# Optimization experiments

Hardware: AMD Instinct MI355X
Metric: run time of the kernel (lower is better)

The kernel has to match this reference:

```python
import jax, jax.numpy as jnp
import numpy as np

B, L, H, N, O = 64, 512, 768, 50, 768
ALPHA = 0.3  # leaky relu slope in GAT
NEG_INF = -9e15


def _position_encoding(n, d):
    # standard sinusoidal PE, shape [n, d]
    pos = jnp.arange(n, dtype=jnp.float32)[:, None]              # [n,1]
    div = jnp.exp(jnp.arange(0, d, 2, dtype=jnp.float32) * (-np.log(10000.0) / d))  # [d/2]
    ang = pos * div[None, :]                                     # [n, d/2]
    return jnp.stack([jnp.sin(ang), jnp.cos(ang)], axis=-1).reshape(n, d)


def _gat_layer(x, adj, W, b, a, ab):
    # Dense GAT layer. Original builds an [N,N,2F] concat tensor then applies
    # linear a; mathematically identical to splitting a into src/dst halves.
    Wh = x @ W + b                                               # [N,F]
    Fdim = Wh.shape[-1]
    a_src = Wh @ a[:Fdim]                                        # [N]
    a_dst = Wh @ a[Fdim:]                                        # [N]
    e = jax.nn.leaky_relu(a_src[:, None] + a_dst[None, :] + ab, negative_slope=ALPHA)
    att = jax.nn.softmax(jnp.where(adj > 0, e, NEG_INF), axis=1)  # rows sum to 1
    return att @ Wh                                              # [N,F]


def setup_inputs() -> dict:
    key = jax.random.key(0)
    ks = jax.random.split(key, 16)
    s = 1.0 / np.sqrt(H)
    utter_embedding = jax.random.normal(ks[0], (B, L, H), jnp.float32)
    cls_ids = jnp.sort(jax.random.randint(ks[1], (B, N), 0, L), axis=1).astype(jnp.int32)
    adj = jax.random.randint(ks[2], (B, N, N), 0, 2).astype(jnp.int32)
    adj = adj | jnp.eye(N, dtype=jnp.int32)  # ensure self loops so softmax rows are valid
    return {
        "utter_embedding": utter_embedding,
        "cls_ids": cls_ids,
        "adj": adj,
        # GAT head 0 (concat=True)
        "W1": jax.random.normal(ks[3], (H, H), jnp.float32) * s,
        "b1": jnp.zeros((H,), jnp.float32),
        "a1": jax.random.normal(ks[4], (2 * H,), jnp.float32) * s,
        "ab1": jnp.zeros((), jnp.float32),
        # GAT out layer (concat=False)
        "W2": jax.random.normal(ks[5], (H, H), jnp.float32) * s,
        "b2": jnp.zeros((H,), jnp.float32),
        "a2": jax.random.normal(ks[6], (2 * H,), jnp.float32) * s,
        "ab2": jnp.zeros((), jnp.float32),
        # Attention pooling over utterances
        "Wa": jax.random.normal(ks[7], (H, H), jnp.float32) * s,
        "ba": jnp.zeros((H,), jnp.float32),
        "v": jax.random.normal(ks[8], (H,), jnp.float32) * s,
        # Final linear
        "Wl": jax.random.normal(ks[9], (H, O), jnp.float32) * s,
        "bl": jnp.zeros((O,), jnp.float32),
    }


def reference(utter_embedding, cls_ids, adj, W1, b1, a1, ab1, W2, b2, a2, ab2,
              Wa, ba, v, Wl, bl):
    pe = _position_encoding(N, H)                                # [N,H]

    def per_dialogue(emb, ids, A):
        # gather [CLS] utterance embeddings: index_select
        x = jnp.take(emb, ids, axis=0)                           # [N,H]
        x = x + pe                                               # position encoder
        # GAT: 1 head concat -> elu, out layer -> elu, residual
        h = jax.nn.elu(_gat_layer(x, A, W1, b1, a1, ab1))
        h = jax.nn.elu(_gat_layer(h, A, W2, b2, a2, ab2)) + x    # residual per GAT.forward
        # attention pooling over N utterances
        scores = jax.nn.softmax(jnp.tanh(h @ Wa + ba) @ v, axis=0)  # [N]
        return scores @ h                                        # [H]

    dialogue = jax.vmap(per_dialogue)(utter_embedding, cls_ids, adj)  # [B,H]
    return dialogue @ Wl + bl                                    # [B,O]
```

## Files before the change

kernel.cpp:

```cpp
#include <hip/hip_runtime.h>
#include <hip/hip_bf16.h>
#include <math.h>

typedef __attribute__((ext_vector_type(8))) short bf16x8;
typedef __attribute__((ext_vector_type(4))) float f32x4;
typedef __attribute__((ext_vector_type(4))) unsigned short u16x4;

constexpr int Bn = 64;
constexpr int Ln = 512;
constexpr int Hd = 768;
constexpr int Nn = 50;
constexpr int On = 768;
constexpr int RP = 64;

__device__ __forceinline__ f32x4 MFMA(bf16x8 a, bf16x8 b, f32x4 c) {
  return __builtin_amdgcn_mfma_f32_16x16x32_bf16(a, b, c, 0, 0, 0);
}
__device__ __forceinline__ unsigned short f2bb(float v) {
  __hip_bfloat16 h = __float2bfloat16(v);
  return *(unsigned short*)&h;
}

struct PrepArgs {
  const float* src[4];
  __hip_bfloat16* dst[4];
  const float* emb;
  const int* ids;
  float* xres;
  __hip_bfloat16* xb;
  float* aux;
};

__global__ __launch_bounds__(256) void prep_kernel(PrepArgs a) {
  int bx = blockIdx.x;
  if (bx < 2304) {
    __shared__ float tile[32][33];
    int job = bx / 576, t = bx % 576;
    const float* W = a.src[job];
    __hip_bfloat16* Wt = a.dst[job];
    int tx = (t % 24) * 32, ty = (t / 24) * 32;
    int c = threadIdx.x & 31, r0 = threadIdx.x >> 5;
    for (int r = r0; r < 32; r += 8)
      tile[r][c] = W[(size_t)(tx + r) * Hd + ty + c];
    __syncthreads();
    for (int r = r0; r < 32; r += 8)
      Wt[(size_t)(ty + r) * Hd + tx + c] = __float2bfloat16(tile[c][r]);
  } else if (bx < 6400) {
    int bn = bx - 2304;
    int b = bn >> 6, i = bn & 63;
    __hip_bfloat16* xbo = a.xb + (size_t)bn * Hd;
    float* xro = a.xres + (size_t)bn * Hd;
    if (i < Nn) {
      int id = a.ids[b * Nn + i];
      const float* src = a.emb + ((size_t)b * Ln + id) * Hd;
      const float kLog = 9.210340371976184f / (float)Hd;
      for (int h = threadIdx.x; h < Hd; h += 256) {
        float freq = expf(-(float)(h & ~1) * kLog);
        float ang = (float)i * freq;
        float v = src[h] + ((h & 1) ? cosf(ang) : sinf(ang));
        xbo[h] = __float2bfloat16(v);
        xro[h] = v;
      }
    } else {
      for (int h = threadIdx.x; h < Hd; h += 256) {
        xbo[h] = __float2bfloat16(0.f);
        xro[h] = 0.f;
      }
    }
  } else {
    int idx = (bx - 6400) * 256 + threadIdx.x;
    if (idx < 5 * Bn * RP) a.aux[idx] = 0.f;
  }
}

template <int EPI>
__global__ __launch_bounds__(256) void gemm_kernel(
    const __hip_bfloat16* __restrict__ A, const __hip_bfloat16* __restrict__ Bt,
    const float* __restrict__ bias, __hip_bfloat16* __restrict__ WhT,
    const float* __restrict__ avec, float* __restrict__ o1,
    float* __restrict__ o2) {
  __shared__ __hip_bfloat16 As[2][64][72];
  __shared__ __hip_bfloat16 Bs[2][64][72];
  int tid = threadIdx.x;
  int wave = tid >> 6, lane = tid & 63;
  int lr = lane & 15, lq = lane >> 4;
  int b = blockIdx.x, col0 = blockIdx.y * 64;
  int row0 = b * RP;
  int sr = tid >> 2, sk = (tid & 3) * 8;
  const __hip_bfloat16* Ap = A + (size_t)(row0 + sr) * Hd + sk;
  const __hip_bfloat16* Bp = Bt + (size_t)(col0 + sr) * Hd + sk;
  uint4 ra0 = *(const uint4*)Ap;
  uint4 ra1 = *(const uint4*)(Ap + 32);
  uint4 rb0 = *(const uint4*)Bp;
  uint4 rb1 = *(const uint4*)(Bp + 32);
  *(uint4*)&As[0][sr][sk] = ra0;
  *(uint4*)&As[0][sr][sk + 32] = ra1;
  *(uint4*)&Bs[0][sr][sk] = rb0;
  *(uint4*)&Bs[0][sr][sk + 32] = rb1;
  f32x4 acc[4] = {};
  __syncthreads();
  int cur = 0;
  for (int kt = 64; kt < Hd; kt += 64) {
    ra0 = *(const uint4*)(Ap + kt);
    ra1 = *(const uint4*)(Ap + kt + 32);
    rb0 = *(const uint4*)(Bp + kt);
    rb1 = *(const uint4*)(Bp + kt + 32);
    bf16x8 af0 = *(const bf16x8*)&As[cur][wave * 16 + lr][lq * 8];
    bf16x8 af1 = *(const bf16x8*)&As[cur][wave * 16 + lr][32 + lq * 8];
#pragma unroll
    for (int ct = 0; ct < 4; ++ct) {
      acc[ct] = MFMA(af0, *(const bf16x8*)&Bs[cur][ct * 16 + lr][lq * 8], acc[ct]);
      acc[ct] = MFMA(af1, *(const bf16x8*)&Bs[cur][ct * 16 + lr][32 + lq * 8], acc[ct]);
    }
    *(uint4*)&As[cur ^ 1][sr][sk] = ra0;
    *(uint4*)&As[cur ^ 1][sr][sk + 32] = ra1;
    *(uint4*)&Bs[cur ^ 1][sr][sk] = rb0;
    *(uint4*)&Bs[cur ^ 1][sr][sk + 32] = rb1;
    __syncthreads();
    cur ^= 1;
  }
  {
    bf16x8 af0 = *(const bf16x8*)&As[cur][wave * 16 + lr][lq * 8];
    bf16x8 af1 = *(const bf16x8*)&As[cur][wave * 16 + lr][32 + lq * 8];
#pragma unroll
    for (int ct = 0; ct < 4; ++ct) {
      acc[ct] = MFMA(af0, *(const bf16x8*)&Bs[cur][ct * 16 + lr][lq * 8], acc[ct]);
      acc[ct] = MFMA(af1, *(const bf16x8*)&Bs[cur][ct * 16 + lr][32 + lq * 8], acc[ct]);
    }
  }
  int lrow0 = wave * 16 + lq * 4;
  if (EPI == 0) {
    float ps[4] = {}, pd[4] = {};
#pragma unroll
    for (int ct = 0; ct < 4; ++ct) {
      int gc = col0 + ct * 16 + lr;
      float bv = bias[gc];
      float a_s = avec[gc], a_d = avec[Hd + gc];
      u16x4 pk;
#pragma unroll
      for (int r = 0; r < 4; ++r) {
        float v = acc[ct][r] + bv;
        pk[r] = f2bb(v);
        ps[r] += v * a_s;
        pd[r] += v * a_d;
      }
      *(u16x4*)(WhT + ((size_t)b * Hd + gc) * RP + lrow0) = pk;
    }
#pragma unroll
    for (int off = 8; off; off >>= 1)
#pragma unroll
      for (int r = 0; r < 4; ++r) {
        ps[r] += __shfl_xor(ps[r], off);
        pd[r] += __shfl_xor(pd[r], off);
      }
    if (lr == 0)
#pragma unroll
      for (int r = 0; r < 4; ++r) {
        int row = lrow0 + r;
        if (row < Nn) {
          atomicAdd(&o1[b * RP + row], ps[r]);
          atomicAdd(&o2[b * RP + row], pd[r]);
        }
      }
  } else {
    float pr[4] = {};
#pragma unroll
    for (int ct = 0; ct < 4; ++ct) {
      int gc = col0 + ct * 16 + lr;
      float bv = bias[gc];
      float vv_ = avec[gc];
#pragma unroll
      for (int r = 0; r < 4; ++r) pr[r] += tanhf(acc[ct][r] + bv) * vv_;
    }
#pragma unroll
    for (int off = 8; off; off >>= 1)
#pragma unroll
      for (int r = 0; r < 4; ++r) pr[r] += __shfl_xor(pr[r], off);
    if (lr == 0)
#pragma unroll
      for (int r = 0; r < 4; ++r) {
        int row = lrow0 + r;
        if (row < Nn) atomicAdd(&o1[b * RP + row], pr[r]);
      }
  }
}

template <int LAYER>
__global__ __launch_bounds__(256) void attf_kernel(
    const float* __restrict__ ssrc, const float* __restrict__ sdst,
    const int* __restrict__ adj, const float* __restrict__ ab,
    const __hip_bfloat16* __restrict__ WhT, const float* __restrict__ xres,
    float* __restrict__ hf, __hip_bfloat16* __restrict__ hb) {
  int b = blockIdx.x / 12, cg = blockIdx.x % 12;
  __shared__ float attL[Nn * 52];
  __shared__ __hip_bfloat16 attB[64 * 72];
  int tid = threadIdx.x;
  float abv = ab[0];
  for (int i = tid; i < 64 * 72; i += 256) attB[i] = __float2bfloat16(0.f);
  for (int idx = tid; idx < Nn * Nn; idx += 256) {
    int i = idx / Nn, j = idx - i * Nn;
    float t = ssrc[b * RP + i] + sdst[b * RP + j] + abv;
    t = t > 0.f ? t : 0.3f * t;
    attL[i * 52 + j] = (adj[(size_t)b * Nn * Nn + idx] > 0) ? t : -9.0e15f;
  }
  __syncthreads();
  if (tid < Nn) {
    float m = -3.0e38f;
    for (int j = 0; j < Nn; ++j) m = fmaxf(m, attL[tid * 52 + j]);
    float s = 0.f;
    for (int j = 0; j < Nn; ++j) {
      float p = expf(attL[tid * 52 + j] - m);
      attL[tid * 52 + j] = p;
      s += p;
    }
    float inv = 1.f / s;
    for (int j = 0; j < Nn; ++j) attL[tid * 52 + j] *= inv;
  }
  __syncthreads();
  for (int idx = tid; idx < Nn * Nn; idx += 256) {
    int i = idx / Nn, j = idx - i * Nn;
    attB[i * 72 + j] = __float2bfloat16(attL[i * 52 + j]);
  }
  __syncthreads();

  int w = tid >> 6, lane = tid & 63, lr = lane & 15, lq = lane >> 4;
  bf16x8 a0 = *(const bf16x8*)&attB[(w * 16 + lr) * 72 + lq * 8];
  bf16x8 a1 = *(const bf16x8*)&attB[(w * 16 + lr) * 72 + 32 + lq * 8];
#pragma unroll
  for (int s = 0; s < 4; ++s) {
    int gc = cg * 64 + s * 16 + lr;
    const __hip_bfloat16* Bp = WhT + ((size_t)b * Hd + gc) * RP + lq * 8;
    f32x4 acc = {};
    acc = MFMA(a0, *(const bf16x8*)Bp, acc);
    acc = MFMA(a1, *(const bf16x8*)(Bp + 32), acc);
#pragma unroll
    for (int r = 0; r < 4; ++r) {
      float v = acc[r];
      v = v > 0.f ? v : expf(v) - 1.f;
      size_t off = ((size_t)b * RP + w * 16 + lq * 4 + r) * Hd + gc;
      if (LAYER == 2) {
        v += xres[off];
        hf[off] = v;
      }
      hb[off] = __float2bfloat16(v);
    }
  }
}

__global__ __launch_bounds__(256) void poolfinal_kernel(
    const float* __restrict__ sraw, const float* __restrict__ h2,
    const __hip_bfloat16* __restrict__ Wlt, const float* __restrict__ bl,
    float* __restrict__ out) {
  int b = blockIdx.x / 3, q = blockIdx.x % 3;
  __shared__ float sc[Nn];
  __shared__ float ds[Hd];
  if (threadIdx.x < 64) {
    int j = threadIdx.x;
    float e = (j < Nn) ? sraw[b * RP + j] : -3.0e38f;
    float m = e;
#pragma unroll
    for (int off = 32; off; off >>= 1) m = fmaxf(m, __shfl_xor(m, off));
    float p = (j < Nn) ? expf(e - m) : 0.f;
    float s = p;
#pragma unroll
    for (int off = 32; off; off >>= 1) s += __shfl_xor(s, off);
    if (j < Nn) sc[j] = p / s;
  }
  __syncthreads();
  for (int h = threadIdx.x; h < Hd; h += 256) {
    float a = 0.f;
#pragma unroll 10
    for (int j = 0; j < Nn; ++j) a += sc[j] * h2[((size_t)b * RP + j) * Hd + h];
    ds[h] = a;
  }
  __syncthreads();
  {
    int o = q * 256 + threadIdx.x;
    float acc = bl[o];
    const uint4* wr = (const uint4*)(Wlt + (size_t)o * Hd);
    for (int kk = 0; kk < Hd / 8; ++kk) {
      union { uint4 u; unsigned short s[8]; } w;
      w.u = wr[kk];
#pragma unroll
      for (int t = 0; t < 8; ++t)
        acc += ds[kk * 8 + t] * __uint_as_float((unsigned)w.s[t] << 16);
    }
    out[(size_t)b * On + o] = acc;
  }
}

extern "C" void kernel_launch(void* const* d_in, const int* in_sizes, int n_in,
                              void* d_out, int out_size, void* d_ws, size_t ws_size,
                              hipStream_t stream) {
  const float* emb = (const float*)d_in[0];
  const int* ids = (const int*)d_in[1];
  const int* adj = (const int*)d_in[2];
  const float* W1 = (const float*)d_in[3];
  const float* b1 = (const float*)d_in[4];
  const float* a1 = (const float*)d_in[5];
  const float* ab1 = (const float*)d_in[6];
  const float* W2 = (const float*)d_in[7];
  const float* b2 = (const float*)d_in[8];
  const float* a2 = (const float*)d_in[9];
  const float* ab2 = (const float*)d_in[10];
  const float* Wa = (const float*)d_in[11];
  const float* ba = (const float*)d_in[12];
  const float* vv = (const float*)d_in[13];
  const float* Wl = (const float*)d_in[14];
  const float* bl = (const float*)d_in[15];
  float* out = (float*)d_out;

  char* p = (char*)d_ws;
  auto alloc = [&](size_t bytes) {
    char* r = p;
    p += (bytes + 255) & ~(size_t)255;
    return r;
  };
  __hip_bfloat16* Wt1 = (__hip_bfloat16*)alloc((size_t)Hd * Hd * 2);
  __hip_bfloat16* Wt2 = (__hip_bfloat16*)alloc((size_t)Hd * Hd * 2);
  __hip_bfloat16* Wta = (__hip_bfloat16*)alloc((size_t)Hd * Hd * 2);
  __hip_bfloat16* Wlt = (__hip_bfloat16*)alloc((size_t)Hd * On * 2);
  float* aux = (float*)alloc((size_t)5 * Bn * RP * 4);
  float* ssrc1 = aux;
  float* sdst1 = aux + Bn * RP;
  float* ssrc2 = aux + 2 * Bn * RP;
  float* sdst2 = aux + 3 * Bn * RP;
  float* sraw = aux + 4 * Bn * RP;
  __hip_bfloat16* xb = (__hip_bfloat16*)alloc((size_t)Bn * RP * Hd * 2);
  float* xres = (float*)alloc((size_t)Bn * RP * Hd * 4);
  __hip_bfloat16* WhT1 = (__hip_bfloat16*)alloc((size_t)Bn * Hd * RP * 2);
  __hip_bfloat16* WhT2 = (__hip_bfloat16*)alloc((size_t)Bn * Hd * RP * 2);
  __hip_bfloat16* h1b = (__hip_bfloat16*)alloc((size_t)Bn * RP * Hd * 2);
  __hip_bfloat16* h2b = (__hip_bfloat16*)alloc((size_t)Bn * RP * Hd * 2);
  float* h2f = (float*)alloc((size_t)Bn * RP * Hd * 4);

  PrepArgs pa;
  pa.src[0] = W1; pa.src[1] = W2; pa.src[2] = Wa; pa.src[3] = Wl;
  pa.dst[0] = Wt1; pa.dst[1] = Wt2; pa.dst[2] = Wta; pa.dst[3] = Wlt;
  pa.emb = emb; pa.ids = ids; pa.xres = xres; pa.xb = xb; pa.aux = aux;
  prep_kernel<<<6480, 256, 0, stream>>>(pa);

  dim3 ggrid(Bn, Hd / 64);
  dim3 agrid(Bn * 12);
  dim3 pgrid(Bn * 3);

  gemm_kernel<0><<<ggrid, 256, 0, stream>>>(xb, Wt1, b1, WhT1, a1, ssrc1, sdst1);
  attf_kernel<1><<<agrid, 256, 0, stream>>>(ssrc1, sdst1, adj, ab1, WhT1,
                                            nullptr, nullptr, h1b);
  gemm_kernel<0><<<ggrid, 256, 0, stream>>>(h1b, Wt2, b2, WhT2, a2, ssrc2, sdst2);
  attf_kernel<2><<<agrid, 256, 0, stream>>>(ssrc2, sdst2, adj, ab2, WhT2, xres,
                                            h2f, h2b);
  gemm_kernel<1><<<ggrid, 256, 0, stream>>>(h2b, Wta, ba, nullptr, vv, sraw,
                                            nullptr);
  poolfinal_kernel<<<pgrid, 256, 0, stream>>>(sraw, h2f, Wlt, bl, out);
}
```

Baseline: 265.8 us.

## Load GEMM MFMA operands directly from global memory, dropping LDS staging

The GEMM kernel no longer stages A and B tiles through double-buffered shared memory with barriers. Each lane now loads its MFMA fragments straight from global memory, relying on L1/L2 caching, inside a fully unrolled K loop. This removes LDS traffic and the per-tile __syncthreads. In exchange, each B row is fetched by all four waves separately and A is fetched by each column block, so global and cache load traffic rises.

```diff
diff --git a/kernel.cpp b/kernel.cpp
--- a/kernel.cpp
+++ b/kernel.cpp
@@ -79,55 +79,33 @@
     const float* __restrict__ bias, __hip_bfloat16* __restrict__ WhT,
     const float* __restrict__ avec, float* __restrict__ o1,
     float* __restrict__ o2) {
-  __shared__ __hip_bfloat16 As[2][64][72];
-  __shared__ __hip_bfloat16 Bs[2][64][72];
   int tid = threadIdx.x;
   int wave = tid >> 6, lane = tid & 63;
   int lr = lane & 15, lq = lane >> 4;
   int b = blockIdx.x, col0 = blockIdx.y * 64;
   int row0 = b * RP;
-  int sr = tid >> 2, sk = (tid & 3) * 8;
-  const __hip_bfloat16* Ap = A + (size_t)(row0 + sr) * Hd + sk;
-  const __hip_bfloat16* Bp = Bt + (size_t)(col0 + sr) * Hd + sk;
-  uint4 ra0 = *(const uint4*)Ap;
-  uint4 ra1 = *(const uint4*)(Ap + 32);
-  uint4 rb0 = *(const uint4*)Bp;
-  uint4 rb1 = *(const uint4*)(Bp + 32);
-  *(uint4*)&As[0][sr][sk] = ra0;
-  *(uint4*)&As[0][sr][sk + 32] = ra1;
-  *(uint4*)&Bs[0][sr][sk] = rb0;
-  *(uint4*)&Bs[0][sr][sk + 32] = rb1;
+
+  const __hip_bfloat16* Ap = A + (size_t)(row0 + wave * 16 + lr) * Hd + lq * 8;
+  const __hip_bfloat16* Bp0 = Bt + (size_t)(col0 + 0 * 16 + lr) * Hd + lq * 8;
+  const __hip_bfloat16* Bp1 = Bt + (size_t)(col0 + 1 * 16 + lr) * Hd + lq * 8;
+  const __hip_bfloat16* Bp2 = Bt + (size_t)(col0 + 2 * 16 + lr) * Hd + lq * 8;
+  const __hip_bfloat16* Bp3 = Bt + (size_t)(col0 + 3 * 16 + lr) * Hd + lq * 8;
+
   f32x4 acc[4] = {};
-  __syncthreads();
-  int cur = 0;
-  for (int kt = 64; kt < Hd; kt += 64) {
-    ra0 = *(const uint4*)(Ap + kt);
-    ra1 = *(const uint4*)(Ap + kt + 32);
-    rb0 = *(const uint4*)(Bp + kt);
-    rb1 = *(const uint4*)(Bp + kt + 32);
-    bf16x8 af0 = *(const bf16x8*)&As[cur][wave * 16 + lr][lq * 8];
-    bf16x8 af1 = *(const bf16x8*)&As[cur][wave * 16 + lr][32 + lq * 8];
-#pragma unroll
-    for (int ct = 0; ct < 4; ++ct) {
-      acc[ct] = MFMA(af0, *(const bf16x8*)&Bs[cur][ct * 16 + lr][lq * 8], acc[ct]);
-      acc[ct] = MFMA(af1, *(const bf16x8*)&Bs[cur][ct * 16 + lr][32 + lq * 8], acc[ct]);
-    }
-    *(uint4*)&As[cur ^ 1][sr][sk] = ra0;
-    *(uint4*)&As[cur ^ 1][sr][sk + 32] = ra1;
-    *(uint4*)&Bs[cur ^ 1][sr][sk] = rb0;
-    *(uint4*)&Bs[cur ^ 1][sr][sk + 32] = rb1;
-    __syncthreads();
-    cur ^= 1;
-  }
-  {
-    bf16x8 af0 = *(const bf16x8*)&As[cur][wave * 16 + lr][lq * 8];
-    bf16x8 af1 = *(const bf16x8*)&As[cur][wave * 16 + lr][32 + lq * 8];
-#pragma unroll
-    for (int ct = 0; ct < 4; ++ct) {
-      acc[ct] = MFMA(af0, *(const bf16x8*)&Bs[cur][ct * 16 + lr][lq * 8], acc[ct]);
-      acc[ct] = MFMA(af1, *(const bf16x8*)&Bs[cur][ct * 16 + lr][32 + lq * 8], acc[ct]);
-    }
-  }
+#pragma unroll
+  for (int kt = 0; kt < Hd; kt += 64) {
+    bf16x8 af0 = *(const bf16x8*)(Ap + kt);
+    bf16x8 af1 = *(const bf16x8*)(Ap + kt + 32);
+    acc[0] = MFMA(af0, *(const bf16x8*)(Bp0 + kt), acc[0]);
+    acc[0] = MFMA(af1, *(const bf16x8*)(Bp0 + kt + 32), acc[0]);
+    acc[1] = MFMA(af0, *(const bf16x8*)(Bp1 + kt), acc[1]);
+    acc[1] = MFMA(af1, *(const bf16x8*)(Bp1 + kt + 32), acc[1]);
+    acc[2] = MFMA(af0, *(const bf16x8*)(Bp2 + kt), acc[2]);
+    acc[2] = MFMA(af1, *(const bf16x8*)(Bp2 + kt + 32), acc[2]);
+    acc[3] = MFMA(af0, *(const bf16x8*)(Bp3 + kt), acc[3]);
+    acc[3] = MFMA(af1, *(const bf16x8*)(Bp3 + kt + 32), acc[3]);
+  }
+
   int lrow0 = wave * 16 + lq * 4;
   if (EPI == 0) {
     float ps[4] = {}, pd[4] = {};
```

New measurement: 349.0 us. +31.3%, slower.
